# Kernel tuning notes

Hardware: AMD Instinct MI355X
Metric: run time of the kernel (lower is better)

Reference implementation:

```python
import jax, jax.numpy as jnp
import numpy as np

NB = 32          # graph_batch_size
NEG_SLOPE = 0.2  # GATv2Conv leaky_relu slope


def _gat_spatial(X, V_Adap, Wl, bl, Wr, br, att, we, gat_bias, Wfc, bfc):
    # X: (B,T,N,F). GATv2 runs per time step on G diagonal blocks of size NB.
    B, T, N, F = X.shape
    G = N // NB
    Xb = X.reshape(B, T, G, NB, F)
    gl = jnp.einsum('btgnf,cf->btgnc', Xb, Wl) + bl  # lin_l (source msgs)
    gr = jnp.einsum('btgnf,cf->btgnc', Xb, Wr) + br  # lin_r (target)
    # diagonal blocks of the learned adjacency logits
    idx = jnp.arange(G)
    Vg = V_Adap[0].reshape(G, NB, G, NB)[idx, :, idx, :]   # (G, j_src, i_tgt)
    attr = jax.nn.sigmoid(Vg)                              # all > 0 => dense edges
    eye = jnp.eye(NB, dtype=bool)
    # PyG: remove self loops, then add self loops with fill_value='mean'
    off = jnp.where(eye, 0.0, attr)
    self_attr = off.sum(axis=1) / (NB - 1)                 # mean incoming per target
    attr_eff = jnp.where(eye, self_attr[:, None, :], attr) # (G, j, i)
    ef = attr_eff[..., None] * we                          # lin_edge, (G,j,i,C)
    ef = jnp.swapaxes(ef, 1, 2)                            # (G,i,j,C)
    # edges only cover flattened node ids 0..NB-1 => attention only for sample 0
    gl0, gr0 = gl[0], gr[0]                                # (T,G,NB,C)
    pre = gl0[:, :, None, :, :] + gr0[:, :, :, None, :] + ef[None]  # (T,G,i,j,C)
    S = jnp.einsum('tgijc,c->tgij', jax.nn.leaky_relu(pre, NEG_SLOPE), att)
    alpha = jax.nn.softmax(S, axis=-1)                     # softmax over sources j
    out0 = jnp.einsum('tgij,tgjc->tgic', alpha, gl0)
    # samples b>0: only the self loop -> alpha=1, message = gl
    out = jnp.concatenate([out0[None], gl[1:]], axis=0) + gat_bias
    y = jnp.einsum('btgnc,oc->btgno', out, Wfc) + bfc      # per-node fc
    return y.reshape(B, T, -1)                             # (B,T,N*spatial_out)


def _lstm_layer(x, Wih, Whh, bih, bhh):
    # torch LSTM gate order: i, f, g, o
    B, T, _ = x.shape
    H = Whh.shape[1]
    xg = jnp.einsum('bti,gi->btg', x, Wih) + bih           # (B,T,4H)
    xg = jnp.swapaxes(xg, 0, 1)                            # (T,B,4H)

    def step(carry, xt):
        h, c = carry
        g = xt + h @ Whh.T + bhh
        i, f, gg, o = jnp.split(g, 4, axis=-1)
        i = jax.nn.sigmoid(i)
        f = jax.nn.sigmoid(f)
        gg = jnp.tanh(gg)
        o = jax.nn.sigmoid(o)
        c = f * c + i * gg
        h = o * jnp.tanh(c)
        return (h, c), h

    h0 = jnp.zeros((B, H), x.dtype)
    _, hs = jax.lax.scan(step, (h0, h0), xg)
    return jnp.swapaxes(hs, 0, 1)                          # (B,T,H)


def setup_inputs() -> dict:
    key = jax.random.key(0)
    ks = jax.random.split(key, 24)
    B, T, N, F = 8, 64, 256, 64
    C, O, NC, H, HL = 128, 32, 16, 1024, 2
    s = 0.05
    inp = {
        'X': jax.random.normal(ks[0], (B, T, N, F), jnp.float32),
        'V_Adap': 0.2 + 0.05 * jax.random.normal(ks[1], (1, N, N), jnp.float32),
        'Wl': s * jax.random.normal(ks[2], (C, F), jnp.float32),
        'bl': s * jax.random.normal(ks[3], (C,), jnp.float32),
        'Wr': s * jax.random.normal(ks[4], (C, F), jnp.float32),
        'br': s * jax.random.normal(ks[5], (C,), jnp.float32),
        'att': s * jax.random.normal(ks[6], (C,), jnp.float32),
        'we': s * jax.random.normal(ks[7], (C,), jnp.float32),
        'gat_bias': s * jax.random.normal(ks[8], (C,), jnp.float32),
        'Wfc': s * jax.random.normal(ks[9], (O, C), jnp.float32),
        'bfc': s * jax.random.normal(ks[10], (O,), jnp.float32),
        'Wih0': s * jax.random.normal(ks[11], (4 * H, N * O), jnp.float32),
        'Whh0': s * jax.random.normal(ks[12], (4 * H, H), jnp.float32),
        'bih0': s * jax.random.normal(ks[13], (4 * H,), jnp.float32),
        'bhh0': s * jax.random.normal(ks[14], (4 * H,), jnp.float32),
        'Wih1': s * jax.random.normal(ks[15], (4 * H, H), jnp.float32),
        'Whh1': s * jax.random.normal(ks[16], (4 * H, H), jnp.float32),
        'bih1': s * jax.random.normal(ks[17], (4 * H,), jnp.float32),
        'bhh1': s * jax.random.normal(ks[18], (4 * H,), jnp.float32),
        'Wout': s * jax.random.normal(ks[19], (NC, H), jnp.float32),
        'bout': s * jax.random.normal(ks[20], (NC,), jnp.float32),
    }
    return inp


def reference(X, V_Adap, Wl, bl, Wr, br, att, we, gat_bias, Wfc, bfc,
              Wih0, Whh0, bih0, bhh0, Wih1, Whh1, bih1, bhh1, Wout, bout):
    s = _gat_spatial(X, V_Adap, Wl, bl, Wr, br, att, we, gat_bias, Wfc, bfc)
    h1 = _lstm_layer(s, Wih0, Whh0, bih0, bhh0)
    h2 = _lstm_layer(h1, Wih1, Whh1, bih1, bhh1)
    return h2[:, -1, :] @ Wout.T + bout                    # (B, num_classes)
```

## Files before the change

### kernel.cpp

```cpp
#include <hip/hip_runtime.h>
#include <cmath>

#define B_ 8
#define T_ 64
#define N_ 256
#define F_ 64
#define C_ 128
#define O_ 32
#define H_ 1024
#define NC_ 16

typedef __attribute__((ext_vector_type(8))) short bf16x8;
typedef __attribute__((ext_vector_type(4))) float f32x4;

__device__ __forceinline__ float sigf(float x){ return 1.f/(1.f+expf(-x)); }

__device__ __forceinline__ unsigned short f2bf(float f){
  unsigned int u = __float_as_uint(f);
  u += 0x7fff + ((u >> 16) & 1);
  return (unsigned short)(u >> 16);
}
__device__ __forceinline__ float bf2f(unsigned short s){
  return __uint_as_float(((unsigned int)s) << 16);
}

__device__ __forceinline__ void gload16(const void* g, void* l){
  __builtin_amdgcn_global_load_lds((const __attribute__((address_space(1))) void*)g,
                                   (__attribute__((address_space(3))) void*)l, 16, 0, 0);
}

__device__ __forceinline__ bf16x8 cvt8(const float* p){
  float4 a = *(const float4*)p, b = *(const float4*)(p + 4);
  bf16x8 r;
  r[0] = (short)f2bf(a.x); r[1] = (short)f2bf(a.y);
  r[2] = (short)f2bf(a.z); r[3] = (short)f2bf(a.w);
  r[4] = (short)f2bf(b.x); r[5] = (short)f2bf(b.y);
  r[6] = (short)f2bf(b.z); r[7] = (short)f2bf(b.w);
  return r;
}

#define FLAGW(l, s, i) ((((l)*65 + (s))*16 + (i)) << 5)
#define NFLAGW 66560

__global__ __launch_bounds__(256) void attr_kernel(const float* __restrict__ V, float* __restrict__ attr){
  __shared__ float sv[32][33];
  __shared__ float selfv[32];
  int g = blockIdx.x, tid = threadIdx.x;
  for (int idx = tid; idx < 1024; idx += 256){
    int j = idx >> 5, i = idx & 31;
    sv[j][i] = sigf(V[(size_t)(g*32 + j)*256 + g*32 + i]);
  }
  __syncthreads();
  if (tid < 32){
    float s = 0.f;
    for (int j = 0; j < 32; ++j) if (j != tid) s += sv[j][tid];
    selfv[tid] = s * (1.f/31.f);
  }
  __syncthreads();
  for (int idx = tid; idx < 1024; idx += 256){
    int j = idx >> 5, i = idx & 31;
    attr[g*1024 + idx] = (j == i) ? selfv[i] : sv[j][i];
  }
}

__global__ __launch_bounds__(256) void prep_kernel(
    const float* __restrict__ Wl, const float* __restrict__ Wr,
    const float* __restrict__ bl, const float* __restrict__ gb,
    const float* __restrict__ Wfc, const float* __restrict__ bfc,
    unsigned short* __restrict__ wcomb,
    float* __restrict__ bias_comb,
    unsigned short* __restrict__ wlr){
  __shared__ float wls[8192], wfcs[4096];
  int tid = threadIdx.x;
  for (int i = tid; i < 8192; i += 256) wls[i] = Wl[i];
  for (int i = tid; i < 4096; i += 256) wfcs[i] = Wfc[i];
  __syncthreads();
  for (int idx = tid; idx < 2048; idx += 256){
    int o = idx >> 6, f = idx & 63;
    float acc = 0.f;
    for (int c = 0; c < 128; ++c) acc = fmaf(wfcs[o*128 + c], wls[c*64 + f], acc);
    wcomb[idx] = f2bf(acc);
  }
  if (tid < 32){
    float acc = bfc[tid];
    for (int c = 0; c < 128; ++c) acc = fmaf(wfcs[tid*128 + c], bl[c] + gb[c], acc);
    bias_comb[tid] = acc;
  }
  for (int idx = tid; idx < 16384; idx += 256){
    int r = idx >> 6, f = idx & 63;
    wlr[idx] = f2bf(r < 128 ? wls[r*64 + f] : Wr[(r-128)*64 + f]);
  }
}

__global__ __launch_bounds__(256) void gemm_proj0(
    const float* __restrict__ X, const unsigned short* __restrict__ wlr,
    const float* __restrict__ bl, const float* __restrict__ br,
    float* __restrict__ gl0, float* __restrict__ gr0){
  int tid = threadIdx.x;
  int lane = tid & 63, w = tid >> 6;
  int lr = lane & 15, ko = lane >> 4;
  int row = blockIdx.x*64 + w*16 + lr;

  bf16x8 af[2];
  #pragma unroll
  for (int ks = 0; ks < 2; ++ks)
    af[ks] = cvt8(&X[(size_t)row*64 + ks*32 + ko*8]);

  f32x4 zero = {0.f,0.f,0.f,0.f};
  #pragma unroll 4
  for (int nt = 0; nt < 16; ++nt){
    f32x4 acc = zero;
    #pragma unroll
    for (int ks = 0; ks < 2; ++ks){
      bf16x8 bv = *(const bf16x8*)&wlr[(size_t)(nt*16 + lr)*64 + ks*32 + ko*8];
      acc = __builtin_amdgcn_mfma_f32_16x16x32_bf16(af[ks], bv, acc, 0, 0, 0);
    }
    int col = nt*16 + lr;
    #pragma unroll
    for (int v = 0; v < 4; ++v){
      int orow = blockIdx.x*64 + w*16 + ko*4 + v;
      if (col < 128) gl0[(size_t)orow*128 + col]        = acc[v] + bl[col];
      else           gr0[(size_t)orow*128 + (col-128)]  = acc[v] + br[col-128];
    }
  }
}

__global__ __launch_bounds__(256) void gemm_rest(
    const float* __restrict__ X, const unsigned short* __restrict__ wcomb,
    const float* __restrict__ bias_comb, unsigned short* __restrict__ xl){
  int tid = threadIdx.x;
  int lane = tid & 63, w = tid >> 6;
  int lr = lane & 15, ko = lane >> 4;
  int r0 = 16384 + blockIdx.x*256 + w*64;

  bf16x8 bv[2][2];
  #pragma unroll
  for (int nt = 0; nt < 2; ++nt)
    #pragma unroll
    for (int ks = 0; ks < 2; ++ks)
      bv[nt][ks] = *(const bf16x8*)&wcomb[(size_t)(nt*16 + lr)*64 + ks*32 + ko*8];

  f32x4 zero = {0.f,0.f,0.f,0.f};
  #pragma unroll
  for (int mt = 0; mt < 4; ++mt){
    int row = r0 + mt*16 + lr;
    bf16x8 af[2];
    #pragma unroll
    for (int ks = 0; ks < 2; ++ks)
      af[ks] = cvt8(&X[(size_t)row*64 + ks*32 + ko*8]);
    f32x4 acc0 = zero, acc1 = zero;
    #pragma unroll
    for (int ks = 0; ks < 2; ++ks){
      acc0 = __builtin_amdgcn_mfma_f32_16x16x32_bf16(af[ks], bv[0][ks], acc0, 0, 0, 0);
      acc1 = __builtin_amdgcn_mfma_f32_16x16x32_bf16(af[ks], bv[1][ks], acc1, 0, 0, 0);
    }
    #pragma unroll
    for (int v = 0; v < 4; ++v){
      int orow = r0 + mt*16 + ko*4 + v;
      xl[(size_t)orow*32 + lr]      = f2bf(acc0[v] + bias_comb[lr]);
      xl[(size_t)orow*32 + 16 + lr] = f2bf(acc1[v] + bias_comb[16 + lr]);
    }
  }
}

__global__ __launch_bounds__(256) void attn_kernel(
    const float* __restrict__ gl0, const float* __restrict__ gr0,
    const float* __restrict__ attr, const float* __restrict__ we, const float* __restrict__ att,
    const float* __restrict__ gbias, const float* __restrict__ Wfc, const float* __restrict__ bfc,
    unsigned short* __restrict__ xl){
  __shared__ float gls[32*129], grs[32*129], os_[32*129], Wfcs[32*129];
  __shared__ float ae[32*33], Ss[32*33];
  __shared__ float wes[128], atts[128];
  int tid = threadIdx.x, blk = blockIdx.x;
  int g = blk & 7, t = blk >> 3;

  const float* glp = gl0 + ((size_t)t*N_ + g*32)*C_;
  const float* grp = gr0 + ((size_t)t*N_ + g*32)*C_;
  for (int idx = tid; idx < 4096; idx += 256){
    int n = idx >> 7, c = idx & 127;
    gls[n*129 + c]  = glp[idx];
    grs[n*129 + c]  = grp[idx];
    Wfcs[n*129 + c] = Wfc[idx];
  }
  for (int idx = tid; idx < 1024; idx += 256) ae[(idx>>5)*33 + (idx&31)] = attr[g*1024 + idx];
  if (tid < 128){ wes[tid] = we[tid]; atts[tid] = att[tid]; }
  __syncthreads();

  int i = tid >> 3, jb = (tid & 7) * 4;
  float a0 = ae[(jb+0)*33 + i], a1 = ae[(jb+1)*33 + i], a2 = ae[(jb+2)*33 + i], a3 = ae[(jb+3)*33 + i];
  float s0 = 0.f, s1 = 0.f, s2 = 0.f, s3 = 0.f;
  for (int cc = 0; cc < 128; ++cc){
    float grv = grs[i*129 + cc];
    float wv = wes[cc], av = atts[cc];
    float p0 = gls[(jb+0)*129 + cc] + grv + a0*wv;
    float p1 = gls[(jb+1)*129 + cc] + grv + a1*wv;
    float p2 = gls[(jb+2)*129 + cc] + grv + a2*wv;
    float p3 = gls[(jb+3)*129 + cc] + grv + a3*wv;
    p0 = p0 > 0.f ? p0 : 0.2f*p0;
    p1 = p1 > 0.f ? p1 : 0.2f*p1;
    p2 = p2 > 0.f ? p2 : 0.2f*p2;
    p3 = p3 > 0.f ? p3 : 0.2f*p3;
    s0 = fmaf(p0, av, s0); s1 = fmaf(p1, av, s1);
    s2 = fmaf(p2, av, s2); s3 = fmaf(p3, av, s3);
  }
  Ss[i*33 + jb + 0] = s0; Ss[i*33 + jb + 1] = s1;
  Ss[i*33 + jb + 2] = s2; Ss[i*33 + jb + 3] = s3;
  __syncthreads();

  if (tid < 32){
    float mx = -1e30f;
    for (int j = 0; j < 32; ++j) mx = fmaxf(mx, Ss[tid*33 + j]);
    float sum = 0.f;
    for (int j = 0; j < 32; ++j) sum += expf(Ss[tid*33 + j] - mx);
    float inv = 1.f / sum;
    for (int j = 0; j < 32; ++j) Ss[tid*33 + j] = expf(Ss[tid*33 + j] - mx) * inv;
  }
  __syncthreads();

  int c2 = tid & 127, ibase = (tid >> 7) * 16;
  float gbv = gbias[c2];
  for (int p = 0; p < 16; ++p){
    int ii = ibase + p;
    float acc = 0.f;
    #pragma unroll
    for (int j = 0; j < 32; ++j) acc = fmaf(Ss[ii*33 + j], gls[j*129 + c2], acc);
    os_[ii*129 + c2] = acc + gbv;
  }
  __syncthreads();

  int o = tid & 31, n2b = tid >> 5;
  float bfv = bfc[o];
  for (int p = 0; p < 4; ++p){
    int n2 = n2b + 8*p;
    float acc = bfv;
    for (int cc = 0; cc < 128; ++cc)
      acc = fmaf(os_[n2*129 + cc], Wfcs[o*129 + cc], acc);
    xl[((size_t)t*N_ + g*32 + n2)*O_ + o] = f2bf(acc);
  }
}

__global__ __launch_bounds__(256) void f2b_kernel(const float* __restrict__ in,
                                                  unsigned short* __restrict__ out, int n4){
  int idx = blockIdx.x*256 + threadIdx.x;
  if (idx >= n4) return;
  float4 v = ((const float4*)in)[idx];
  ushort4 o;
  o.x = f2bf(v.x); o.y = f2bf(v.y); o.z = f2bf(v.z); o.w = f2bf(v.w);
  ((ushort4*)out)[idx] = o;
}

__global__ __launch_bounds__(256) void w2cat_kernel(const float* __restrict__ Whh1,
                                                    const float* __restrict__ Wih1,
                                                    unsigned short* __restrict__ w2){
  int row = blockIdx.x, tid = threadIdx.x;
  const float* a = Whh1 + (size_t)row*1024 + tid*4;
  const float* b = Wih1 + (size_t)row*1024 + tid*4;
  float4 va = *(const float4*)a, vb = *(const float4*)b;
  ushort4 oa, ob;
  oa.x = f2bf(va.x); oa.y = f2bf(va.y); oa.z = f2bf(va.z); oa.w = f2bf(va.w);
  ob.x = f2bf(vb.x); ob.y = f2bf(vb.y); ob.z = f2bf(vb.z); ob.w = f2bf(vb.w);
  *(ushort4*)&w2[(size_t)row*2048 + tid*4]        = oa;
  *(ushort4*)&w2[(size_t)row*2048 + 1024 + tid*4] = ob;
}

__global__ __launch_bounds__(256) void gemm_bf2s(
    const unsigned short* __restrict__ A, const unsigned short* __restrict__ W,
    float* __restrict__ Yp, int N, int K){
  __shared__ __align__(16) short As[2][64*64];
  __shared__ __align__(16) short Bs[2][128*64];
  int tid = threadIdx.x;
  int id = blockIdx.x;
  int ks = id >> 8, rest = id & 255;
  int xcd = rest & 7, local = rest >> 3;
  int nt = xcd*4 + (local & 3), mt = local >> 2;
  int m0 = mt*64, n0 = nt*128;
  int kbase = ks * (K >> 1);
  float* Y = Yp + (size_t)ks*512*N;
  int lane = tid & 63;
  int w = tid >> 6, wm = w >> 1, wn = w & 1;
  int lr = lane & 15, ko = lane >> 4;
  int wbase = tid & ~63;

  auto STAGE = [&](int buf, int kc){
    #pragma unroll
    for (int it = 0; it < 2; ++it){
      int chunk = it*256 + tid;
      int r = chunk >> 3, c8 = chunk & 7;
      int cs = (c8 ^ (r & 7)) << 3;
      gload16(&A[(size_t)(m0 + r)*K + kc + cs], &As[buf][(size_t)(it*256 + wbase)*8]);
    }
    #pragma unroll
    for (int it = 0; it < 4; ++it){
      int chunk = it*256 + tid;
      int r = chunk >> 3, c8 = chunk & 7;
      int cs = (c8 ^ (r & 7)) << 3;
      gload16(&W[(size_t)(n0 + r)*K + kc + cs], &Bs[buf][(size_t)(it*256 + wbase)*8]);
    }
  };

  f32x4 zero = {0.f,0.f,0.f,0.f};
  f32x4 acc[2][4] = {{zero,zero,zero,zero},{zero,zero,zero,zero}};

  STAGE(0, kbase);
  __syncthreads();
  int nk = K >> 7;
  for (int kt = 0; kt < nk; ++kt){
    int cur = kt & 1;
    if (kt + 1 < nk) STAGE(cur ^ 1, kbase + ((kt + 1) << 6));
    #pragma unroll
    for (int kk = 0; kk < 2; ++kk){
      int s = kk*4 + ko;
      bf16x8 af[2], bfv[4];
      #pragma unroll
      for (int m = 0; m < 2; ++m){
        int row = wm*32 + m*16 + lr;
        af[m] = *(const bf16x8*)&As[cur][row*64 + ((s ^ (row & 7)) << 3)];
      }
      #pragma unroll
      for (int n = 0; n < 4; ++n){
        int row = wn*64 + n*16 + lr;
        bfv[n] = *(const bf16x8*)&Bs[cur][row*64 + ((s ^ (row & 7)) << 3)];
      }
      #pragma unroll
      for (int m = 0; m < 2; ++m)
        #pragma unroll
        for (int n = 0; n < 4; ++n)
          acc[m][n] = __builtin_amdgcn_mfma_f32_16x16x32_bf16(af[m], bfv[n], acc[m][n], 0, 0, 0);
    }
    __syncthreads();
  }

  #pragma unroll
  for (int m = 0; m < 2; ++m)
    #pragma unroll
    for (int n = 0; n < 4; ++n)
      #pragma unroll
      for (int v = 0; v < 4; ++v){
        int row = m0 + wm*32 + m*16 + ko*4 + v;
        int col = n0 + wn*64 + n*16 + lr;
        Y[(size_t)row*N + col] = acc[m][n][v];
      }
}

__global__ __launch_bounds__(256) void ksum_kernel(
    const float* __restrict__ p0, const float* __restrict__ p1,
    const float* __restrict__ b1, const float* __restrict__ b2,
    float* __restrict__ Y, unsigned* __restrict__ syncw){
  int idx = blockIdx.x*256 + threadIdx.x;
  if (idx < NFLAGW) syncw[idx] = 0u;
  int i4 = idx;
  float4 a = ((const float4*)p0)[i4];
  float4 b = ((const float4*)p1)[i4];
  int col = (i4 << 2) & 4095;
  float4 u = *(const float4*)&b1[col];
  float4 v = *(const float4*)&b2[col];
  float4 o;
  o.x = a.x + b.x + u.x + v.x;
  o.y = a.y + b.y + u.y + v.y;
  o.z = a.z + b.z + u.z + v.z;
  o.w = a.w + b.w + u.w + v.w;
  ((float4*)Y)[i4] = o;
}

__global__ __launch_bounds__(512) void lstm_persist(
    const unsigned short* __restrict__ whh0,
    const unsigned short* __restrict__ w2cat,
    const float* __restrict__ xg0,
    const float* __restrict__ bih1, const float* __restrict__ bhh1,
    unsigned short* __restrict__ h1seq,
    unsigned short* __restrict__ h2seq,
    unsigned* __restrict__ syncw){
  __shared__ float red[4][8][64];
  const int tid = threadIdx.x;
  const int lane = tid & 63, w = tid >> 6;
  const int g = w >> 2, ws = w & 3;
  const bool layer2 = (blockIdx.x >= 128);
  const int lb = layer2 ? (int)blockIdx.x - 128 : (int)blockIdx.x;
  const int lr = lane & 15, ko = lane >> 4;
  const int q = lr >> 2, dl = lr & 3;
  const int row = q*H_ + lb*8 + g*4 + dl;

  bf16x8 wreg[16];
  if (!layer2){
    const unsigned short* wrow = whh0 + (size_t)row*1024 + ws*256;
    #pragma unroll
    for (int kk = 0; kk < 8; ++kk) wreg[kk] = *(const bf16x8*)&wrow[kk*32 + ko*8];
  } else {
    const unsigned short* wrow = w2cat + (size_t)row*2048 + ws*512;
    #pragma unroll
    for (int kk = 0; kk < 16; ++kk) wreg[kk] = *(const bf16x8*)&wrow[kk*32 + ko*8];
  }

  const int g2 = tid >> 5, bt = (tid >> 2) & 7, dl2 = tid & 3;
  const int dimt = lb*8 + g2*4 + dl2;
  float creg = 0.f;
  float b2r[4] = {0.f,0.f,0.f,0.f};
  if (layer2 && tid < 64){
    #pragma unroll
    for (int qq = 0; qq < 4; ++qq) b2r[qq] = bih1[qq*H_ + dimt] + bhh1[qq*H_ + dimt];
  }
  const bf16x8 zero8 = {0,0,0,0,0,0,0,0};
  const int ttend = layer2 ? 64 : 63;

  for (int tt = 0; tt <= ttend; ++tt){
    const int tau = layer2 ? tt - 1 : tt;
    const bool active = layer2 ? (tt >= 1) : true;

    if (w == 0){
      int s1 = -1, s2 = -1;
      if (!layer2){ if (tt > 0) s1 = tt - 1; }
      else if (tt >= 1){ s1 = tau; s2 = tau - 1; }
      if (s1 >= 0){
        unsigned* p1 = syncw + FLAGW(0, s1, lane & 15);
        unsigned* p2 = (s2 >= 0) ? (syncw + FLAGW(1, s2, lane & 15)) : (unsigned*)0;
        for (;;){
          unsigned v = 8u;
          if (lane < 16)            v = __hip_atomic_load(p1, __ATOMIC_RELAXED, __HIP_MEMORY_SCOPE_AGENT);
          else if (lane < 32 && p2) v = __hip_atomic_load(p2, __ATOMIC_RELAXED, __HIP_MEMORY_SCOPE_AGENT);
          if (__all(v >= 8u)) break;
          __builtin_amdgcn_s_sleep(1);
        }
      }
    }
    __syncthreads();

    f32x4 accv = {0.f,0.f,0.f,0.f};
    if (active){
      const unsigned short* arow = nullptr;
      if (!layer2){
        if (tt > 0) arow = h1seq + ((size_t)(lr & 7)*T_ + (tt-1))*H_ + ws*256;
      } else {
        if (ws < 2){ if (tau > 0) arow = h2seq + ((size_t)(lr & 7)*T_ + (tau-1))*H_ + ws*512; }
        else         arow = h1seq + ((size_t)(lr & 7)*T_ + tau)*H_ + (ws-2)*512;
      }
      if (arow){
        f32x4 acc2 = {0.f,0.f,0.f,0.f};
        if (!layer2){
          #pragma unroll
          for (int kk = 0; kk < 8; ++kk){
            bf16x8 av = (lr < 8) ? *(const bf16x8*)&arow[kk*32 + ko*8] : zero8;
            if (kk & 1) acc2 = __builtin_amdgcn_mfma_f32_16x16x32_bf16(av, wreg[kk], acc2, 0, 0, 0);
            else        accv = __builtin_amdgcn_mfma_f32_16x16x32_bf16(av, wreg[kk], accv, 0, 0, 0);
          }
        } else {
          #pragma unroll
          for (int kk = 0; kk < 16; ++kk){
            bf16x8 av = (lr < 8) ? *(const bf16x8*)&arow[kk*32 + ko*8] : zero8;
            if (kk & 1) acc2 = __builtin_amdgcn_mfma_f32_16x16x32_bf16(av, wreg[kk], acc2, 0, 0, 0);
            else        accv = __builtin_amdgcn_mfma_f32_16x16x32_bf16(av, wreg[kk], accv, 0, 0, 0);
          }
        }
        accv = accv + acc2;
      }
    }
    #pragma unroll
    for (int v = 0; v < 4; ++v) red[v][w][lane] = accv[v];
    __syncthreads();

    if (active && tid < 64){
      float pre[4];
      #pragma unroll
      for (int qq = 0; qq < 4; ++qq){
        int lsrc = (bt >> 2)*16 + qq*4 + dl2, v = bt & 3;
        pre[qq] = red[v][g2*4+0][lsrc] + red[v][g2*4+1][lsrc]
                + red[v][g2*4+2][lsrc] + red[v][g2*4+3][lsrc];
      }
      float pi, pf, pg, po;
      if (!layer2){
        size_t xb = ((size_t)bt*T_ + tt)*4096;
        pi = pre[0] + xg0[xb + 0*H_ + dimt];
        pf = pre[1] + xg0[xb + 1*H_ + dimt];
        pg = pre[2] + xg0[xb + 2*H_ + dimt];
        po = pre[3] + xg0[xb + 3*H_ + dimt];
      } else {
        pi = pre[0] + b2r[0]; pf = pre[1] + b2r[1];
        pg = pre[2] + b2r[2]; po = pre[3] + b2r[3];
      }
      float i_ = sigf(pi), f_ = sigf(pf), g_ = tanhf(pg), o_ = sigf(po);
      float cn = fmaf(f_, creg, i_*g_);
      creg = cn;
      float hn = o_ * tanhf(cn);
      unsigned short* hp = (layer2 ? h2seq : h1seq) + ((size_t)bt*T_ + tau)*H_ + dimt;
      __hip_atomic_store(hp, f2bf(hn), __ATOMIC_RELAXED, __HIP_MEMORY_SCOPE_AGENT);
    }
    __syncthreads();

    if (active && tid == 0){
      const int fl = layer2 ? 1 : 0;
      const int s  = layer2 ? tau : tt;
      __hip_atomic_fetch_add(syncw + FLAGW(fl, s, lb & 15), 1u,
                             __ATOMIC_RELAXED, __HIP_MEMORY_SCOPE_AGENT);
    }
  }
}

__global__ __launch_bounds__(128) void final_kernel(
    const unsigned short* __restrict__ h2_seq, const float* __restrict__ Wout,
    const float* __restrict__ bout, float* __restrict__ out){
  int tid = threadIdx.x;
  int b = tid >> 4, nc = tid & 15;
  const unsigned short* hp = h2_seq + ((size_t)b*T_ + (T_ - 1))*H_;
  const float* wp = Wout + nc*H_;
  float acc = bout[nc];
  for (int k = 0; k < 1024; ++k) acc = fmaf(bf2f(hp[k]), wp[k], acc);
  out[tid] = acc;
}

extern "C" void kernel_launch(void* const* d_in, const int* in_sizes, int n_in,
                              void* d_out, int out_size, void* d_ws, size_t ws_size,
                              hipStream_t stream){
  const float* X    = (const float*)d_in[0];
  const float* V    = (const float*)d_in[1];
  const float* Wl   = (const float*)d_in[2];
  const float* bl   = (const float*)d_in[3];
  const float* Wr   = (const float*)d_in[4];
  const float* br   = (const float*)d_in[5];
  const float* att  = (const float*)d_in[6];
  const float* we   = (const float*)d_in[7];
  const float* gb   = (const float*)d_in[8];
  const float* Wfc  = (const float*)d_in[9];
  const float* bfc  = (const float*)d_in[10];
  const float* Wih0 = (const float*)d_in[11];
  const float* Whh0 = (const float*)d_in[12];
  const float* bih0 = (const float*)d_in[13];
  const float* bhh0 = (const float*)d_in[14];
  const float* Wih1 = (const float*)d_in[15];
  const float* Whh1 = (const float*)d_in[16];
  const float* bih1 = (const float*)d_in[17];
  const float* bhh1 = (const float*)d_in[18];
  const float* Wout = (const float*)d_in[19];
  const float* bout = (const float*)d_in[20];

  float* ws   = (float*)d_ws;
  float* attr = ws;
  float* gl0  = attr + 8192;
  float* gr0  = gl0 + 2097152;
  float* xg0  = gr0 + 2097152;
  float* bias_comb = xg0 + 2097152;
  unsigned short* xl_bf  = (unsigned short*)(bias_comb + 64);
  unsigned short* w0_bf  = xl_bf + 4194304;
  unsigned short* wh0_bf = w0_bf + 33554432;
  unsigned short* w2_bf  = wh0_bf + 4194304;
  unsigned short* h1_bf  = w2_bf + 8388608;
  unsigned short* h2_bf  = h1_bf + 524288;
  unsigned short* wlr_bf = h2_bf + 524288;
  unsigned short* wcomb  = wlr_bf + 16384;
  unsigned* syncw = (unsigned*)xl_bf;
  (void)in_sizes; (void)n_in; (void)out_size; (void)ws_size;

  attr_kernel<<<8, 256, 0, stream>>>(V, attr);
  prep_kernel<<<1, 256, 0, stream>>>(Wl, Wr, bl, gb, Wfc, bfc, wcomb, bias_comb, wlr_bf);
  gemm_proj0<<<256, 256, 0, stream>>>(X, wlr_bf, bl, br, gl0, gr0);
  attn_kernel<<<512, 256, 0, stream>>>(gl0, gr0, attr, we, att, gb, Wfc, bfc, xl_bf);
  gemm_rest<<<448, 256, 0, stream>>>(X, wcomb, bias_comb, xl_bf);

  f2b_kernel<<<32768, 256, 0, stream>>>(Wih0, w0_bf, 8388608);
  f2b_kernel<<<4096, 256, 0, stream>>>(Whh0, wh0_bf, 1048576);
  w2cat_kernel<<<4096, 256, 0, stream>>>(Whh1, Wih1, w2_bf);

  gemm_bf2s<<<512, 256, 0, stream>>>(xl_bf, w0_bf, gl0, 4096, 8192);
  ksum_kernel<<<2048, 256, 0, stream>>>(gl0, gr0, bih0, bhh0, xg0, syncw);

  {
    void* args[] = {(void*)&wh0_bf, (void*)&w2_bf, (void*)&xg0,
                    (void*)&bih1, (void*)&bhh1, (void*)&h1_bf, (void*)&h2_bf,
                    (void*)&syncw};
    hipLaunchCooperativeKernel((const void*)lstm_persist, dim3(256), dim3(512),
                               args, 0, stream);
  }

  final_kernel<<<1, 128, 0, stream>>>(h2_bf, Wout, bout, (float*)d_out);
}
```

Baseline: 600.9 us.

## Halve persistent LSTM grid: 16 hidden dims per block, 2-way K split

The persistent two-layer LSTM kernel now runs on 128 blocks instead of 256. Each block covers 16 hidden dimensions per layer with a 2-way K split across waves instead of 4-way, which doubles the weights kept in registers per wave. The step flag threshold drops from 8 to 4 to match the smaller number of blocks per layer. The aim is to cut grid-wide synchronisation and cross-wave reduction cost per timestep, at the cost of longer serial MFMA chains per wave and heavy register pressure (32 bf16x8 vectors in layer 2), which may cause spills.

```diff
diff --git a/kernel.cpp b/kernel.cpp
--- a/kernel.cpp
+++ b/kernel.cpp
@@ -41,6 +41,8 @@
 
 #define FLAGW(l, s, i) ((((l)*65 + (s))*16 + (i)) << 5)
 #define NFLAGW 66560
+#define LBLK 64
+#define FLAG_THRESH 4u
 
 __global__ __launch_bounds__(256) void attr_kernel(const float* __restrict__ V, float* __restrict__ attr){
   __shared__ float sv[32][33];
@@ -373,29 +375,30 @@
   __shared__ float red[4][8][64];
   const int tid = threadIdx.x;
   const int lane = tid & 63, w = tid >> 6;
-  const int g = w >> 2, ws = w & 3;
-  const bool layer2 = (blockIdx.x >= 128);
-  const int lb = layer2 ? (int)blockIdx.x - 128 : (int)blockIdx.x;
+  const int g = w >> 1, ws = w & 1;
+  const bool layer2 = (blockIdx.x >= LBLK);
+  const int lb = layer2 ? (int)blockIdx.x - LBLK : (int)blockIdx.x;
   const int lr = lane & 15, ko = lane >> 4;
   const int q = lr >> 2, dl = lr & 3;
-  const int row = q*H_ + lb*8 + g*4 + dl;
-
-  bf16x8 wreg[16];
+  const int row = q*H_ + lb*16 + g*4 + dl;
+
+  bf16x8 wreg1[16];
+  bf16x8 wreg2[32];
   if (!layer2){
-    const unsigned short* wrow = whh0 + (size_t)row*1024 + ws*256;
-    #pragma unroll
-    for (int kk = 0; kk < 8; ++kk) wreg[kk] = *(const bf16x8*)&wrow[kk*32 + ko*8];
+    const unsigned short* wrow = whh0 + (size_t)row*1024 + ws*512;
+    #pragma unroll
+    for (int kk = 0; kk < 16; ++kk) wreg1[kk] = *(const bf16x8*)&wrow[kk*32 + ko*8];
   } else {
-    const unsigned short* wrow = w2cat + (size_t)row*2048 + ws*512;
-    #pragma unroll
-    for (int kk = 0; kk < 16; ++kk) wreg[kk] = *(const bf16x8*)&wrow[kk*32 + ko*8];
+    const unsigned short* wrow = w2cat + (size_t)row*2048 + ws*1024;
+    #pragma unroll
+    for (int kk = 0; kk < 32; ++kk) wreg2[kk] = *(const bf16x8*)&wrow[kk*32 + ko*8];
   }
 
   const int g2 = tid >> 5, bt = (tid >> 2) & 7, dl2 = tid & 3;
-  const int dimt = lb*8 + g2*4 + dl2;
+  const int dimt = lb*16 + g2*4 + dl2;
   float creg = 0.f;
   float b2r[4] = {0.f,0.f,0.f,0.f};
-  if (layer2 && tid < 64){
+  if (layer2 && tid < 128){
     #pragma unroll
     for (int qq = 0; qq < 4; ++qq) b2r[qq] = bih1[qq*H_ + dimt] + bhh1[qq*H_ + dimt];
   }
@@ -414,10 +417,10 @@
         unsigned* p1 = syncw + FLAGW(0, s1, lane & 15);
         unsigned* p2 = (s2 >= 0) ? (syncw + FLAGW(1, s2, lane & 15)) : (unsigned*)0;
         for (;;){
-          unsigned v = 8u;
+          unsigned v = FLAG_THRESH;
           if (lane < 16)            v = __hip_atomic_load(p1, __ATOMIC_RELAXED, __HIP_MEMORY_SCOPE_AGENT);
           else if (lane < 32 && p2) v = __hip_atomic_load(p2, __ATOMIC_RELAXED, __HIP_MEMORY_SCOPE_AGENT);
-          if (__all(v >= 8u)) break;
+          if (__all(v >= FLAG_THRESH)) break;
           __builtin_amdgcn_s_sleep(1);
         }
       }
@@ -428,26 +431,26 @@
     if (active){
       const unsigned short* arow = nullptr;
       if (!layer2){
-        if (tt > 0) arow = h1seq + ((size_t)(lr & 7)*T_ + (tt-1))*H_ + ws*256;
+        if (tt > 0) arow = h1seq + ((size_t)(lr & 7)*T_ + (tt-1))*H_ + ws*512;
       } else {
-        if (ws < 2){ if (tau > 0) arow = h2seq + ((size_t)(lr & 7)*T_ + (tau-1))*H_ + ws*512; }
-        else         arow = h1seq + ((size_t)(lr & 7)*T_ + tau)*H_ + (ws-2)*512;
+        if (ws == 0){ if (tau > 0) arow = h2seq + ((size_t)(lr & 7)*T_ + (tau-1))*H_; }
+        else          arow = h1seq + ((size_t)(lr & 7)*T_ + tau)*H_;
       }
       if (arow){
         f32x4 acc2 = {0.f,0.f,0.f,0.f};
         if (!layer2){
           #pragma unroll
-          for (int kk = 0; kk < 8; ++kk){
+          for (int kk = 0; kk < 16; ++kk){
             bf16x8 av = (lr < 8) ? *(const bf16x8*)&arow[kk*32 + ko*8] : zero8;
-            if (kk & 1) acc2 = __builtin_amdgcn_mfma_f32_16x16x32_bf16(av, wreg[kk], acc2, 0, 0, 0);
-            else        accv = __builtin_amdgcn_mfma_f32_16x16x32_bf16(av, wreg[kk], accv, 0, 0, 0);
+            if (kk & 1) acc2 = __builtin_amdgcn_mfma_f32_16x16x32_bf16(av, wreg1[kk], acc2, 0, 0, 0);
+            else        accv = __builtin_amdgcn_mfma_f32_16x16x32_bf16(av, wreg1[kk], accv, 0, 0, 0);
           }
         } else {
           #pragma unroll
-          for (int kk = 0; kk < 16; ++kk){
+          for (int kk = 0; kk < 32; ++kk){
             bf16x8 av = (lr < 8) ? *(const bf16x8*)&arow[kk*32 + ko*8] : zero8;
-            if (kk & 1) acc2 = __builtin_amdgcn_mfma_f32_16x16x32_bf16(av, wreg[kk], acc2, 0, 0, 0);
-            else        accv = __builtin_amdgcn_mfma_f32_16x16x32_bf16(av, wreg[kk], accv, 0, 0, 0);
+            if (kk & 1) acc2 = __builtin_amdgcn_mfma_f32_16x16x32_bf16(av, wreg2[kk], acc2, 0, 0, 0);
+            else        accv = __builtin_amdgcn_mfma_f32_16x16x32_bf16(av, wreg2[kk], accv, 0, 0, 0);
           }
         }
         accv = accv + acc2;
@@ -457,13 +460,12 @@
     for (int v = 0; v < 4; ++v) red[v][w][lane] = accv[v];
     __syncthreads();
 
-    if (active && tid < 64){
+    if (active && tid < 128){
       float pre[4];
       #pragma unroll
       for (int qq = 0; qq < 4; ++qq){
         int lsrc = (bt >> 2)*16 + qq*4 + dl2, v = bt & 3;
-        pre[qq] = red[v][g2*4+0][lsrc] + red[v][g2*4+1][lsrc]
-                + red[v][g2*4+2][lsrc] + red[v][g2*4+3][lsrc];
+        pre[qq] = red[v][g2*2+0][lsrc] + red[v][g2*2+1][lsrc];
       }
       float pi, pf, pg, po;
       if (!layer2){
@@ -565,7 +567,7 @@
     void* args[] = {(void*)&wh0_bf, (void*)&w2_bf, (void*)&xg0,
                     (void*)&bih1, (void*)&bhh1, (void*)&h1_bf, (void*)&h2_bf,
                     (void*)&syncw};
-    hipLaunchCooperativeKernel((const void*)lstm_persist, dim3(256), dim3(512),
+    hipLaunchCooperativeKernel((const void*)lstm_persist, dim3(128), dim3(512),
                                args, 0, stream);
   }
 
```

Measured after the change: 824.6 us. +37.2%, slower.

## Replace per-step counter barriers with per-block progress tags and per-wave waits

Applied to the files above, without the earlier changes.

Swaps the shared per-step fetch-add counters for one monotonic progress tag per block. Each wave polls only the tags of the producer blocks whose hidden-state slice it actually reads, instead of one wave waiting on all flags and then block-wide syncing. The reduction buffer is double-buffered by step parity so two __syncthreads per step can be dropped, and wave 0 publishes its tag right after its own h stores drain. This is meant to cut serialization and barrier latency in the persistent LSTM recurrence. The trade-off is more polling traffic and reliance on relaxed atomics plus an explicit vmcnt wait for ordering.

```diff
diff --git a/kernel.cpp b/kernel.cpp
--- a/kernel.cpp
+++ b/kernel.cpp
@@ -39,8 +39,8 @@
   return r;
 }
 
-#define FLAGW(l, s, i) ((((l)*65 + (s))*16 + (i)) << 5)
-#define NFLAGW 66560
+#define TAGW(l, b) ((((l)*128) + (b)) << 5)
+#define NTAGW 8192
 
 __global__ __launch_bounds__(256) void attr_kernel(const float* __restrict__ V, float* __restrict__ attr){
   __shared__ float sv[32][33];
@@ -347,7 +347,7 @@
     const float* __restrict__ b1, const float* __restrict__ b2,
     float* __restrict__ Y, unsigned* __restrict__ syncw){
   int idx = blockIdx.x*256 + threadIdx.x;
-  if (idx < NFLAGW) syncw[idx] = 0u;
+  if (idx < NTAGW) syncw[idx] = 0u;
   int i4 = idx;
   float4 a = ((const float4*)p0)[i4];
   float4 b = ((const float4*)p1)[i4];
@@ -370,7 +370,7 @@
     unsigned short* __restrict__ h1seq,
     unsigned short* __restrict__ h2seq,
     unsigned* __restrict__ syncw){
-  __shared__ float red[4][8][64];
+  __shared__ float red[2][4][8][64];
   const int tid = threadIdx.x;
   const int lane = tid & 63, w = tid >> 6;
   const int g = w >> 2, ws = w & 3;
@@ -405,24 +405,25 @@
   for (int tt = 0; tt <= ttend; ++tt){
     const int tau = layer2 ? tt - 1 : tt;
     const bool active = layer2 ? (tt >= 1) : true;
-
-    if (w == 0){
-      int s1 = -1, s2 = -1;
-      if (!layer2){ if (tt > 0) s1 = tt - 1; }
-      else if (tt >= 1){ s1 = tau; s2 = tau - 1; }
-      if (s1 >= 0){
-        unsigned* p1 = syncw + FLAGW(0, s1, lane & 15);
-        unsigned* p2 = (s2 >= 0) ? (syncw + FLAGW(1, s2, lane & 15)) : (unsigned*)0;
+    const int par = tt & 1;
+
+    {
+      int base = -1, cnt = 0, need = 0;
+      if (!layer2){
+        if (tt > 0){ base = ws*32; cnt = 32; need = tt; }
+      } else if (tt >= 1){
+        if (ws < 2){ if (tau >= 1){ base = 128 + ws*64; cnt = 64; need = tau; } }
+        else        {               base = (ws-2)*64;   cnt = 64; need = tau+1; }
+      }
+      if (base >= 0){
+        unsigned* tp = syncw + ((size_t)(base + (lane & (cnt-1))) << 5);
         for (;;){
-          unsigned v = 8u;
-          if (lane < 16)            v = __hip_atomic_load(p1, __ATOMIC_RELAXED, __HIP_MEMORY_SCOPE_AGENT);
-          else if (lane < 32 && p2) v = __hip_atomic_load(p2, __ATOMIC_RELAXED, __HIP_MEMORY_SCOPE_AGENT);
-          if (__all(v >= 8u)) break;
+          unsigned v = __hip_atomic_load(tp, __ATOMIC_RELAXED, __HIP_MEMORY_SCOPE_AGENT);
+          if (__all(v >= (unsigned)need)) break;
           __builtin_amdgcn_s_sleep(1);
         }
       }
     }
-    __syncthreads();
 
     f32x4 accv = {0.f,0.f,0.f,0.f};
     if (active){
@@ -454,16 +455,16 @@
       }
     }
     #pragma unroll
-    for (int v = 0; v < 4; ++v) red[v][w][lane] = accv[v];
+    for (int v = 0; v < 4; ++v) red[par][v][w][lane] = accv[v];
     __syncthreads();
 
-    if (active && tid < 64){
+    if (active && w == 0){
       float pre[4];
       #pragma unroll
       for (int qq = 0; qq < 4; ++qq){
         int lsrc = (bt >> 2)*16 + qq*4 + dl2, v = bt & 3;
-        pre[qq] = red[v][g2*4+0][lsrc] + red[v][g2*4+1][lsrc]
-                + red[v][g2*4+2][lsrc] + red[v][g2*4+3][lsrc];
+        pre[qq] = red[par][v][g2*4+0][lsrc] + red[par][v][g2*4+1][lsrc]
+                + red[par][v][g2*4+2][lsrc] + red[par][v][g2*4+3][lsrc];
       }
       float pi, pf, pg, po;
       if (!layer2){
@@ -482,14 +483,12 @@
       float hn = o_ * tanhf(cn);
       unsigned short* hp = (layer2 ? h2seq : h1seq) + ((size_t)bt*T_ + tau)*H_ + dimt;
       __hip_atomic_store(hp, f2bf(hn), __ATOMIC_RELAXED, __HIP_MEMORY_SCOPE_AGENT);
-    }
-    __syncthreads();
-
-    if (active && tid == 0){
-      const int fl = layer2 ? 1 : 0;
-      const int s  = layer2 ? tau : tt;
-      __hip_atomic_fetch_add(syncw + FLAGW(fl, s, lb & 15), 1u,
-                             __ATOMIC_RELAXED, __HIP_MEMORY_SCOPE_AGENT);
+      asm volatile("s_waitcnt vmcnt(0)" ::: "memory");
+      if (lane == 0){
+        const int fl = layer2 ? 1 : 0;
+        __hip_atomic_store(syncw + TAGW(fl, lb), (unsigned)((layer2 ? tau : tt) + 1),
+                           __ATOMIC_RELAXED, __HIP_MEMORY_SCOPE_AGENT);
+      }
     }
   }
 }
```

After: 660.8 us. +10.0%, slower.

## Replace per-step counter flags with per-block monotonic step tags in persistent LSTM

Applied to the files above, without the earlier changes.

Inter-block synchronization in the persistent LSTM kernel moves from per-(layer,step,group) atomic counters, each polled until it reaches 8, to one monotonically increasing step tag per block. Consumers poll all 128 producer tags per layer in parallel across the lanes of the first wave. The final __syncthreads and the separate fetch_add are removed: wave 0 waits on vmcnt and stores its tag directly after writing h. This shortens the per-step critical path and shrinks the flag buffer that has to be zeroed, but each poll now reads more flags, and it depends on ordering the h stores before the tag store using only relaxed atomics plus a waitcnt.

```diff
diff --git a/kernel.cpp b/kernel.cpp
--- a/kernel.cpp
+++ b/kernel.cpp
@@ -39,8 +39,8 @@
   return r;
 }
 
-#define FLAGW(l, s, i) ((((l)*65 + (s))*16 + (i)) << 5)
-#define NFLAGW 66560
+#define TAGW(i) ((i) << 5)
+#define NTAGW 8192
 
 __global__ __launch_bounds__(256) void attr_kernel(const float* __restrict__ V, float* __restrict__ attr){
   __shared__ float sv[32][33];
@@ -347,7 +347,7 @@
     const float* __restrict__ b1, const float* __restrict__ b2,
     float* __restrict__ Y, unsigned* __restrict__ syncw){
   int idx = blockIdx.x*256 + threadIdx.x;
-  if (idx < NFLAGW) syncw[idx] = 0u;
+  if (idx < NTAGW) syncw[idx] = 0u;
   int i4 = idx;
   float4 a = ((const float4*)p0)[i4];
   float4 b = ((const float4*)p1)[i4];
@@ -400,24 +400,29 @@
     for (int qq = 0; qq < 4; ++qq) b2r[qq] = bih1[qq*H_ + dimt] + bhh1[qq*H_ + dimt];
   }
   const bf16x8 zero8 = {0,0,0,0,0,0,0,0};
-  const int ttend = layer2 ? 64 : 63;
-
-  for (int tt = 0; tt <= ttend; ++tt){
+  const int tt0 = layer2 ? 1 : 0;
+  const int tt1 = layer2 ? 64 : 63;
+
+  for (int tt = tt0; tt <= tt1; ++tt){
     const int tau = layer2 ? tt - 1 : tt;
-    const bool active = layer2 ? (tt >= 1) : true;
 
     if (w == 0){
-      int s1 = -1, s2 = -1;
-      if (!layer2){ if (tt > 0) s1 = tt - 1; }
-      else if (tt >= 1){ s1 = tau; s2 = tau - 1; }
-      if (s1 >= 0){
-        unsigned* p1 = syncw + FLAGW(0, s1, lane & 15);
-        unsigned* p2 = (s2 >= 0) ? (syncw + FLAGW(1, s2, lane & 15)) : (unsigned*)0;
+      const bool poll1 = layer2 || (tt > 0);
+      if (poll1){
+        const unsigned need1 = (unsigned)tt;
+        const unsigned need2 = (unsigned)(tt - 1);
+        unsigned* pa = syncw + TAGW(lane);
+        unsigned* pb = syncw + TAGW(64 + lane);
+        unsigned* pc = syncw + TAGW(128 + lane);
+        unsigned* pd = syncw + TAGW(192 + lane);
+        const bool poll2 = layer2 && (tt >= 2);
         for (;;){
-          unsigned v = 8u;
-          if (lane < 16)            v = __hip_atomic_load(p1, __ATOMIC_RELAXED, __HIP_MEMORY_SCOPE_AGENT);
-          else if (lane < 32 && p2) v = __hip_atomic_load(p2, __ATOMIC_RELAXED, __HIP_MEMORY_SCOPE_AGENT);
-          if (__all(v >= 8u)) break;
+          bool ok = (__hip_atomic_load(pa, __ATOMIC_RELAXED, __HIP_MEMORY_SCOPE_AGENT) >= need1)
+                 && (__hip_atomic_load(pb, __ATOMIC_RELAXED, __HIP_MEMORY_SCOPE_AGENT) >= need1);
+          if (poll2)
+            ok = ok && (__hip_atomic_load(pc, __ATOMIC_RELAXED, __HIP_MEMORY_SCOPE_AGENT) >= need2)
+                    && (__hip_atomic_load(pd, __ATOMIC_RELAXED, __HIP_MEMORY_SCOPE_AGENT) >= need2);
+          if (__all(ok)) break;
           __builtin_amdgcn_s_sleep(1);
         }
       }
@@ -425,7 +430,7 @@
     __syncthreads();
 
     f32x4 accv = {0.f,0.f,0.f,0.f};
-    if (active){
+    {
       const unsigned short* arow = nullptr;
       if (!layer2){
         if (tt > 0) arow = h1seq + ((size_t)(lr & 7)*T_ + (tt-1))*H_ + ws*256;
@@ -457,7 +462,7 @@
     for (int v = 0; v < 4; ++v) red[v][w][lane] = accv[v];
     __syncthreads();
 
-    if (active && tid < 64){
+    if (w == 0){
       float pre[4];
       #pragma unroll
       for (int qq = 0; qq < 4; ++qq){
@@ -482,14 +487,10 @@
       float hn = o_ * tanhf(cn);
       unsigned short* hp = (layer2 ? h2seq : h1seq) + ((size_t)bt*T_ + tau)*H_ + dimt;
       __hip_atomic_store(hp, f2bf(hn), __ATOMIC_RELAXED, __HIP_MEMORY_SCOPE_AGENT);
-    }
-    __syncthreads();
-
-    if (active && tid == 0){
-      const int fl = layer2 ? 1 : 0;
-      const int s  = layer2 ? tau : tt;
-      __hip_atomic_fetch_add(syncw + FLAGW(fl, s, lb & 15), 1u,
-                             __ATOMIC_RELAXED, __HIP_MEMORY_SCOPE_AGENT);
+      asm volatile("s_waitcnt vmcnt(0)" ::: "memory");
+      if (lane == 0)
+        __hip_atomic_store(syncw + TAGW((layer2 ? 128 : 0) + lb), (unsigned)(tau + 1),
+                           __ATOMIC_RELAXED, __HIP_MEMORY_SCOPE_AGENT);
     }
   }
 }
```

Result: slower. 639.8 us (+6.5%).
